# Performance work log

Hardware: AMD Instinct MI355X
Metric: run time of the kernel (lower is better)

Reference implementation:

```python
import jax, jax.numpy as jnp
import numpy as np

jax.config.update("jax_enable_x64", True)  # loss accumulates int64 squared index diffs (~1e14)

PATCH, STRIDE = 7, 1


def extract_patches(img, p, s):
    # img: [b, c, h, w] -> patches [b, N, c*p*p], N = oh*ow (normalize_patch='none')
    pat = jax.lax.conv_general_dilated_patches(img, (p, p), (s, s), 'VALID')  # [b, c*p*p, oh, ow]
    b, d = pat.shape[0], pat.shape[1]
    return pat.reshape(b, d, -1).transpose(0, 2, 1)


def bisect_left(a, v):
    # Exact replica of np.searchsorted(a, v, side='left') binary search,
    # applied (as in the original code) to an UNSORTED int array `a`.
    # a: [N] int, v: [M] int -> [M] insertion indices in [0, N].
    N = a.shape[0]
    lo = jnp.zeros(v.shape, jnp.int64)
    hi = jnp.full(v.shape, N, jnp.int64)
    n_iter = int(np.ceil(np.log2(N))) + 1
    for _ in range(n_iter):
        mid = (lo + hi) // 2
        am = a[jnp.clip(mid, 0, N - 1)]
        go = lo < hi
        pred = am < v
        lo = jnp.where(go & pred, mid + 1, lo)
        hi = jnp.where(go & (~pred), mid, hi)
    return lo


def nearest_vals(a, v):
    # Vectorized find_nearest(a, v_i) for all v_i. a: [N], v: [M].
    N = a.shape[0]
    idx = bisect_left(a, v)
    a_prev = a[jnp.clip(idx - 1, 0, N - 1)]
    a_at = a[jnp.clip(idx, 0, N - 1)]
    take_prev = (idx > 0) & ((idx == N) | (jnp.abs(v - a_prev) < jnp.abs(v - a_at)))
    return jnp.where(take_prev, a_prev, a_at)


def reference(x, y, rand):
    # rand: [b, d, num_proj]; per-batch projection matrix, normalized by unbiased column std
    rand = rand / jnp.std(rand, axis=1, keepdims=True, ddof=1)
    xp = extract_patches(x, PATCH, STRIDE)  # [b, N, d]
    yp = extract_patches(y, PATCH, STRIDE)  # [b, N, d]
    proj_x = jnp.einsum('bnd,bdp->bnp', xp, rand)
    proj_y = jnp.einsum('bnd,bdp->bnp', yp, rand)
    # Original overwrites projections with argsort indices; only j=0 is used
    # because of the early return inside the projection loop.
    ai = jnp.argsort(proj_x[:, :, 0], axis=1).astype(jnp.int64)  # [b, N]
    at = jnp.argsort(proj_y[:, :, 0], axis=1).astype(jnp.int64)  # [b, N]
    nearest = jax.vmap(nearest_vals)(at, ai)  # [b, N]
    N = ai.shape[1]
    per_image = jnp.sum((ai - nearest) ** 2, axis=1) / N  # int sum -> float
    return jnp.mean(per_image)  # batch_reduction='mean'


def setup_inputs() -> dict:
    key = jax.random.key(0)
    k1, k2, k3 = jax.random.split(key, 3)
    b, c, h, w = 4, 3, 256, 256
    d = c * PATCH * PATCH  # 147
    x = jax.random.normal(k1, (b, c, h, w), dtype=jnp.float32)
    y = jax.random.normal(k2, (b, c, h, w), dtype=jnp.float32)
    rand = jax.random.normal(k3, (b, d, 1), dtype=jnp.float32)
    return {"x": x, "y": y, "rand": rand}
```

## Files before the change

### kernel.cpp

```cpp
#include <hip/hip_runtime.h>
#include <stdint.h>

#define OH 250
#define OW 250
#define NPTS (OH*OW)
#define NSEG 4
#define D 147
#define CH 3
#define IMH 256
#define IMW 256
#define NITER 17
#define NBUCK 8192
#define CAP 128
#define SIG0 12.124355652982141
#define LT 12

typedef unsigned long long u64;
typedef unsigned int u32;

#define OFF_SREC  0UL
#define OFF_A     33554432UL
#define OFF_CTRL  34554432UL
#define OFF_CURS  34554432UL
#define OFF_SUMS  34685504UL
#define OFF_TICK  34685536UL
#define OFF_OFLOW 34685544UL
#define CTRL_LEN  131116UL
#define OFF_BASES 34685548UL
#define WS_NEED   34816636UL

__device__ __forceinline__ u64 packd(double f) {
  u64 u = (u64)__double_as_longlong(f);
  return (u & 0x8000000000000000ULL) ? ~u : (u | 0x8000000000000000ULL);
}

__device__ __forceinline__ int bucket_of(u64 rec) {
  u64 t = rec & ~0x1FFFFULL;
  u64 bits = (t & 0x8000000000000000ULL) ? (t & 0x7FFFFFFFFFFFFFFFULL) : ~t;
  double v = __longlong_as_double((long long)bits);
  double z = (v + 4.0 * SIG0) * ((double)NBUCK / (8.0 * SIG0));
  int b = (z <= 0.0) ? 0 : (int)z;
  if (b > NBUCK - 1) b = NBUCK - 1;
  return b;
}

__global__ __launch_bounds__(256) void conv_kern(const float* __restrict__ y,
                                                 const float* __restrict__ rnd,
                                                 u64* __restrict__ srec,
                                                 u32* __restrict__ curs,
                                                 u32* __restrict__ oflow) {
  __shared__ float tile[CH][22][22];
  __shared__ double w[D];
  int b = blockIdx.z;
  const float* in = y + (size_t)b * CH * IMH * IMW;
  int bi = blockIdx.y * 16, bj = blockIdx.x * 16;
  int tid = threadIdx.y * 16 + threadIdx.x;
  int lane = tid & 63;

  {
    double v0 = (double)rnd[b * D + lane];
    double v1 = (double)rnd[b * D + lane + 64];
    double v2 = (lane + 128 < D) ? (double)rnd[b * D + lane + 128] : 0.0;
    double sm = v0 + v1 + v2;
    #pragma unroll
    for (int o = 32; o > 0; o >>= 1) sm += __shfl_xor(sm, o, 64);
    double mean = sm / (double)D;
    double d0 = v0 - mean, d1 = v1 - mean;
    double d2 = (lane + 128 < D) ? (v2 - mean) : 0.0;
    double ss = d0 * d0 + d1 * d1 + d2 * d2;
    #pragma unroll
    for (int o = 32; o > 0; o >>= 1) ss += __shfl_xor(ss, o, 64);
    double stdv = sqrt(ss / (double)(D - 1));
    w[lane] = v0 / stdv;
    w[lane + 64] = v1 / stdv;
    if (lane + 128 < D) w[lane + 128] = v2 / stdv;
  }
  for (int c = 0; c < CH; ++c)
    for (int t = tid; t < 22 * 22; t += 256) {
      int rr = t / 22, cc = t - rr * 22;
      int r = bi + rr, col = bj + cc;
      float v = 0.f;
      if (r < IMH && col < IMW) v = in[((size_t)c * IMH + r) * IMW + col];
      tile[c][rr][cc] = v;
    }
  __syncthreads();
  int i = bi + threadIdx.y, j = bj + threadIdx.x;
  if (i < OH && j < OW) {
    double acc = 0.0;
    #pragma unroll
    for (int c = 0; c < CH; ++c)
      #pragma unroll
      for (int ph = 0; ph < 7; ++ph)
        #pragma unroll
        for (int pw = 0; pw < 7; ++pw)
          acc = fma((double)tile[c][threadIdx.y + ph][threadIdx.x + pw],
                    w[c * 49 + ph * 7 + pw], acc);
    int n = i * OW + j;
    u64 rec = (packd(acc) & ~0x1FFFFULL) | (u64)(u32)n;
    int bk = b * NBUCK + bucket_of(rec);
    u32 pos = atomicAdd(&curs[bk], 1u);
    if (pos < CAP) srec[(size_t)bk * CAP + pos] = rec;
    else atomicOr(oflow, 1u);
  }
}

__global__ __launch_bounds__(1024) void scan_kern(const u32* __restrict__ curs,
                                                  u32* __restrict__ bases,
                                                  u32* __restrict__ oflow) {
  __shared__ u32 part[1024];
  int seg = blockIdx.x, t = threadIdx.x;
  u32 c[8]; u32 run = 0;
  #pragma unroll
  for (int m = 0; m < 8; ++m) {
    u32 v = curs[seg * NBUCK + 8 * t + m];
    c[m] = v > CAP ? CAP : v;
    run += c[m];
  }
  part[t] = run;
  __syncthreads();
  for (int off = 1; off < 1024; off <<= 1) {
    u32 v = (t >= off) ? part[t - off] : 0u;
    __syncthreads();
    part[t] += v;
    __syncthreads();
  }
  u32 ex = part[t] - run;
  #pragma unroll
  for (int m = 0; m < 8; ++m) {
    bases[seg * (NBUCK + 1) + 8 * t + m] = ex;
    ex += c[m];
  }
  if (t == 1023) {
    bases[seg * (NBUCK + 1) + NBUCK] = ex;
    if (ex != NPTS) atomicOr(oflow, 2u);
  }
}

__global__ __launch_bounds__(512) void bsort_kern(const u64* __restrict__ srec,
                                                  const u32* __restrict__ bases,
                                                  u32* __restrict__ a) {
  __shared__ u64 buf[8][CAP];
  int wid = threadIdx.x >> 6, lane = threadIdx.x & 63;
  int B = blockIdx.x * 8 + wid;
  int seg = B / NBUCK, bk = B & (NBUCK - 1);
  u32 b0 = bases[seg * (NBUCK + 1) + bk];
  u32 b1 = bases[seg * (NBUCK + 1) + bk + 1];
  int n = (int)(b1 - b0);
  const u64* src = srec + (size_t)B * CAP;
  u32* dst = a + (size_t)seg * NPTS + b0;
  for (int i = lane; i < n; i += 64) buf[wid][i] = src[i];
  __syncthreads();
  for (int i = lane; i < n; i += 64) {
    u64 x = buf[wid][i];
    int r = 0;
    for (int j = 0; j < n; ++j) r += (buf[wid][j] < x);
    dst[r] = (u32)(x & 0x1FFFFULL);
  }
}

__global__ __launch_bounds__(256) void loss_kern(const u32* __restrict__ a_all,
                                                 u64* __restrict__ sums,
                                                 u32* __restrict__ tick,
                                                 const u32* __restrict__ oflow,
                                                 float* __restrict__ out,
                                                 int nblocks) {
  __shared__ u32 tval[1 << LT];
  __shared__ u64 parts[4];
  __shared__ u32 rank_s;
  int tid = threadIdx.x;
  int seg = blockIdx.y;
  const u32* A = a_all + (size_t)seg * NPTS;
  for (int h = 1 + tid; h < (1 << LT); h += 256) {
    int d = 31 - __clz(h);
    int lo = 0, hi = NPTS;
    for (int k = d - 1; k >= 0; --k) {
      int mid = (lo + hi) >> 1;
      if (lo < hi) { if ((h >> k) & 1) lo = mid + 1; else hi = mid; }
    }
    int pos = (lo + hi) >> 1;
    if (pos > NPTS - 1) pos = NPTS - 1;
    tval[h] = A[pos];
  }
  __syncthreads();

  int v = blockIdx.x * 256 + tid;
  u64 tsum = 0;
  if (v < NPTS) {
    int lo = 0, hi = NPTS, h = 1;
    #pragma unroll
    for (int it = 0; it < LT; ++it) {
      int am = (int)tval[h];
      bool pred = am < v;
      if (lo < hi) {
        int mid = (lo + hi) >> 1;
        if (pred) lo = mid + 1; else hi = mid;
      }
      h = 2 * h + (pred ? 1 : 0);
    }
    #pragma unroll
    for (int it = LT; it < NITER; ++it) {
      int mid = (lo + hi) >> 1;
      int cm = mid > NPTS - 1 ? NPTS - 1 : mid;
      int am = (int)A[cm];
      if (lo < hi) { if (am < v) lo = mid + 1; else hi = mid; }
    }
    int pi = lo - 1; if (pi < 0) pi = 0; if (pi > NPTS - 1) pi = NPTS - 1;
    int ci = lo;     if (ci > NPTS - 1) ci = NPTS - 1;
    int ap = (int)A[pi], aa = (int)A[ci];
    int d1 = v - ap; if (d1 < 0) d1 = -d1;
    int d2 = v - aa; if (d2 < 0) d2 = -d2;
    bool tp = (lo > 0) && ((lo == NPTS) || (d1 < d2));
    long long dd = (long long)(v - (tp ? ap : aa));
    tsum = (u64)(dd * dd);
  }
  for (int off = 32; off > 0; off >>= 1) tsum += __shfl_down(tsum, off, 64);
  int lane = tid & 63, wid = tid >> 6;
  if (lane == 0) parts[wid] = tsum;
  __syncthreads();
  if (tid == 0) {
    u64 bsum = parts[0] + parts[1] + parts[2] + parts[3];
    u64 old = atomicAdd(&sums[seg], bsum);
    asm volatile("" : : "v"(old) : "memory");
    rank_s = atomicAdd(&tick[1], 1u);
    if (rank_s == (u32)(nblocks - 1)) {
      u32 of = __hip_atomic_load(oflow, __ATOMIC_RELAXED, __HIP_MEMORY_SCOPE_AGENT);
      if (of) { out[0] = 8.0e12f + 1.0e11f * (float)of; return; }
      double l = 0.0;
      for (int s = 0; s < NSEG; ++s) {
        u64 sv = __hip_atomic_load(&sums[s], __ATOMIC_RELAXED, __HIP_MEMORY_SCOPE_AGENT);
        l += (double)(long long)sv / (double)NPTS;
      }
      out[0] = (float)(l / 4.0);
    }
  }
}

__global__ void guard_kern(float* __restrict__ out) {
  if (threadIdx.x == 0 && blockIdx.x == 0) out[0] = 9.0e12f;
}

extern "C" void kernel_launch(void* const* d_in, const int* in_sizes, int n_in,
                              void* d_out, int out_size, void* d_ws, size_t ws_size,
                              hipStream_t stream) {
  (void)in_sizes; (void)n_in; (void)out_size;
  if (ws_size < WS_NEED) { guard_kern<<<1, 64, 0, stream>>>((float*)d_out); return; }
  const float* y   = (const float*)d_in[1];
  const float* rnd = (const float*)d_in[2];

  char* ws = (char*)d_ws;
  u64* srec   = (u64*)(ws + OFF_SREC);
  u32* aidx   = (u32*)(ws + OFF_A);
  u32* curs   = (u32*)(ws + OFF_CURS);
  u64* sums   = (u64*)(ws + OFF_SUMS);
  u32* tick   = (u32*)(ws + OFF_TICK);
  u32* oflow  = (u32*)(ws + OFF_OFLOW);
  u32* bases  = (u32*)(ws + OFF_BASES);
  float* out  = (float*)d_out;

  hipMemsetAsync(ws + OFF_CTRL, 0, CTRL_LEN, stream);
  conv_kern<<<dim3(16, 16, NSEG), dim3(16, 16), 0, stream>>>(y, rnd, srec, curs, oflow);
  scan_kern<<<NSEG, 1024, 0, stream>>>(curs, bases, oflow);
  bsort_kern<<<NSEG * NBUCK / 8, 512, 0, stream>>>(srec, bases, aidx);
  int nb = 245 * NSEG;
  loss_kern<<<dim3(245, NSEG), 256, 0, stream>>>(aidx, sums, tick, oflow, out, nb);
}
```

Measured before the change: 146.3 us.

## Process two queries per thread in loss kernel and shrink cached search tree

The loss kernel now has each thread run two independent binary searches, for v and v+31250, interleaving their loads. This halves the grid and gives each thread more memory-level parallelism. The shared-memory implicit tree drops from 12 to 8 levels, which makes the tree-building prologue much cheaper but adds global loads to every search. The conv kernel also keeps a separate accumulator per channel, shortening the serial fma dependency chain slightly at the cost of changed summation order, which could in rare cases alter a tie in the sort keys.

New measurement: 122.9 us. 1.19x faster.

```diff
diff --git a/kernel.cpp b/kernel.cpp
--- a/kernel.cpp
+++ b/kernel.cpp
@@ -13,7 +13,8 @@
 #define NBUCK 8192
 #define CAP 128
 #define SIG0 12.124355652982141
-#define LT 12
+#define LT 8
+#define HSEG 31250
 
 typedef unsigned long long u64;
 typedef unsigned int u32;
@@ -88,13 +89,16 @@
   if (i < OH && j < OW) {
     double acc = 0.0;
     #pragma unroll
-    for (int c = 0; c < CH; ++c)
+    for (int c = 0; c < CH; ++c) {
+      double ac = 0.0;
       #pragma unroll
       for (int ph = 0; ph < 7; ++ph)
         #pragma unroll
         for (int pw = 0; pw < 7; ++pw)
-          acc = fma((double)tile[c][threadIdx.y + ph][threadIdx.x + pw],
-                    w[c * 49 + ph * 7 + pw], acc);
+          ac = fma((double)tile[c][threadIdx.y + ph][threadIdx.x + pw],
+                   w[c * 49 + ph * 7 + pw], ac);
+      acc += ac;
+    }
     int n = i * OW + j;
     u64 rec = (packd(acc) & ~0x1FFFFULL) | (u64)(u32)n;
     int bk = b * NBUCK + bucket_of(rec);
@@ -183,35 +187,53 @@
   }
   __syncthreads();
 
-  int v = blockIdx.x * 256 + tid;
+  int v0 = blockIdx.x * 256 + tid;
+  int v1 = v0 + HSEG;
+  bool act = v0 < HSEG;
+  int lo0 = 0, hi0 = NPTS, h0 = 1;
+  int lo1 = 0, hi1 = NPTS, h1 = 1;
+  #pragma unroll
+  for (int it = 0; it < LT; ++it) {
+    int am0 = (int)tval[h0];
+    int am1 = (int)tval[h1];
+    bool p0 = am0 < v0, p1 = am1 < v1;
+    if (lo0 < hi0) { int mid = (lo0 + hi0) >> 1; if (p0) lo0 = mid + 1; else hi0 = mid; }
+    if (lo1 < hi1) { int mid = (lo1 + hi1) >> 1; if (p1) lo1 = mid + 1; else hi1 = mid; }
+    h0 = 2 * h0 + (p0 ? 1 : 0);
+    h1 = 2 * h1 + (p1 ? 1 : 0);
+  }
+  #pragma unroll
+  for (int it = LT; it < NITER; ++it) {
+    int mid0 = (lo0 + hi0) >> 1, mid1 = (lo1 + hi1) >> 1;
+    int cm0 = mid0 > NPTS - 1 ? NPTS - 1 : mid0;
+    int cm1 = mid1 > NPTS - 1 ? NPTS - 1 : mid1;
+    int am0 = (int)A[cm0];
+    int am1 = (int)A[cm1];
+    if (lo0 < hi0) { if (am0 < v0) lo0 = mid0 + 1; else hi0 = mid0; }
+    if (lo1 < hi1) { if (am1 < v1) lo1 = mid1 + 1; else hi1 = mid1; }
+  }
   u64 tsum = 0;
-  if (v < NPTS) {
-    int lo = 0, hi = NPTS, h = 1;
-    #pragma unroll
-    for (int it = 0; it < LT; ++it) {
-      int am = (int)tval[h];
-      bool pred = am < v;
-      if (lo < hi) {
-        int mid = (lo + hi) >> 1;
-        if (pred) lo = mid + 1; else hi = mid;
-      }
-      h = 2 * h + (pred ? 1 : 0);
-    }
-    #pragma unroll
-    for (int it = LT; it < NITER; ++it) {
-      int mid = (lo + hi) >> 1;
-      int cm = mid > NPTS - 1 ? NPTS - 1 : mid;
-      int am = (int)A[cm];
-      if (lo < hi) { if (am < v) lo = mid + 1; else hi = mid; }
-    }
-    int pi = lo - 1; if (pi < 0) pi = 0; if (pi > NPTS - 1) pi = NPTS - 1;
-    int ci = lo;     if (ci > NPTS - 1) ci = NPTS - 1;
-    int ap = (int)A[pi], aa = (int)A[ci];
-    int d1 = v - ap; if (d1 < 0) d1 = -d1;
-    int d2 = v - aa; if (d2 < 0) d2 = -d2;
-    bool tp = (lo > 0) && ((lo == NPTS) || (d1 < d2));
-    long long dd = (long long)(v - (tp ? ap : aa));
-    tsum = (u64)(dd * dd);
+  if (act) {
+    {
+      int pi = lo0 - 1; if (pi < 0) pi = 0; if (pi > NPTS - 1) pi = NPTS - 1;
+      int ci = lo0;     if (ci > NPTS - 1) ci = NPTS - 1;
+      int ap = (int)A[pi], aa = (int)A[ci];
+      int d1 = v0 - ap; if (d1 < 0) d1 = -d1;
+      int d2 = v0 - aa; if (d2 < 0) d2 = -d2;
+      bool tp = (lo0 > 0) && ((lo0 == NPTS) || (d1 < d2));
+      long long dd = (long long)(v0 - (tp ? ap : aa));
+      tsum += (u64)(dd * dd);
+    }
+    {
+      int pi = lo1 - 1; if (pi < 0) pi = 0; if (pi > NPTS - 1) pi = NPTS - 1;
+      int ci = lo1;     if (ci > NPTS - 1) ci = NPTS - 1;
+      int ap = (int)A[pi], aa = (int)A[ci];
+      int d1 = v1 - ap; if (d1 < 0) d1 = -d1;
+      int d2 = v1 - aa; if (d2 < 0) d2 = -d2;
+      bool tp = (lo1 > 0) && ((lo1 == NPTS) || (d1 < d2));
+      long long dd = (long long)(v1 - (tp ? ap : aa));
+      tsum += (u64)(dd * dd);
+    }
   }
   for (int off = 32; off > 0; off >>= 1) tsum += __shfl_down(tsum, off, 64);
   int lane = tid & 63, wid = tid >> 6;
@@ -261,6 +283,6 @@
   conv_kern<<<dim3(16, 16, NSEG), dim3(16, 16), 0, stream>>>(y, rnd, srec, curs, oflow);
   scan_kern<<<NSEG, 1024, 0, stream>>>(curs, bases, oflow);
   bsort_kern<<<NSEG * NBUCK / 8, 512, 0, stream>>>(srec, bases, aidx);
-  int nb = 245 * NSEG;
-  loss_kern<<<dim3(245, NSEG), 256, 0, stream>>>(aidx, sums, tick, oflow, out, nb);
-}
+  int nbx = (HSEG + 255) / 256;
+  loss_kern<<<dim3(nbx, NSEG), 256, 0, stream>>>(aidx, sums, tick, oflow, out, nbx * NSEG);
+}
```
